# Performance work log

Hardware: AMD Instinct MI355X
Metric: run time of the kernel (lower is better)

The kernel has to match this reference:

```python
import jax, jax.numpy as jnp
import numpy as np

D_MODEL = 1024
NUM_HEADS = 16
HEAD_DIM = D_MODEL // NUM_HEADS


def setup_inputs() -> dict:
    key = jax.random.key(0)
    ks = jax.random.split(key, 9)
    s = 1.0 / np.sqrt(D_MODEL)
    inp = {
        "x": jax.random.normal(ks[0], (4, 2048, D_MODEL), dtype=jnp.float32),
        "wq": jax.random.uniform(ks[1], (D_MODEL, D_MODEL), jnp.float32, -s, s),
        "bq": jax.random.uniform(ks[2], (D_MODEL,), jnp.float32, -s, s),
        "wk": jax.random.uniform(ks[3], (D_MODEL, D_MODEL), jnp.float32, -s, s),
        "bk": jax.random.uniform(ks[4], (D_MODEL,), jnp.float32, -s, s),
        "wv": jax.random.uniform(ks[5], (D_MODEL, D_MODEL), jnp.float32, -s, s),
        "bv": jax.random.uniform(ks[6], (D_MODEL,), jnp.float32, -s, s),
        "wo": jax.random.uniform(ks[7], (D_MODEL, D_MODEL), jnp.float32, -s, s),
        "bo": jax.random.uniform(ks[8], (D_MODEL,), jnp.float32, -s, s),
    }
    return inp


def _split_heads(t):
    # [B, S, D] -> [B, H, S, Dh]
    b, s, _ = t.shape
    return t.reshape(b, s, NUM_HEADS, HEAD_DIM).transpose(0, 2, 1, 3)


def reference(x, wq, bq, wk, bk, wv, bv, wo, bo):
    b, s, _ = x.shape
    q = _split_heads(x @ wq.T + bq)
    k = _split_heads(x @ wk.T + bk)
    v = _split_heads(x @ wv.T + bv)
    scale = 1.0 / np.sqrt(HEAD_DIM).astype(np.float32)
    scores = jnp.einsum('bhqd,bhkd->bhqk', q, k) * scale  # [B,H,S,S]
    probs = jax.nn.softmax(scores, axis=-1)
    ctx = jnp.einsum('bhqk,bhkd->bhqd', probs, v)  # [B,H,S,Dh]
    ctx = ctx.transpose(0, 2, 1, 3).reshape(b, s, D_MODEL)
    return ctx @ wo.T + bo
```

## Files before the change

### kernel.cpp

```cpp
#include <hip/hip_runtime.h>
#include <stdint.h>

typedef short bf16x8 __attribute__((ext_vector_type(8)));
typedef float f32x4 __attribute__((ext_vector_type(4)));

#define D_MODEL 1024
#define NHEAD   16
#define HDIM    64
#define BATCH   4
#define SEQ     2048
#define NTOK    (BATCH * SEQ)

#define BM 128
#define BN 128
#define BK 64

#define LOG2E 1.44269504088896340736f

__device__ __forceinline__ unsigned short f2bf(float f) {
  unsigned int u = __float_as_uint(f);
  u += 0x7fff + ((u >> 16) & 1);
  return (unsigned short)(u >> 16);
}

__device__ __forceinline__ void gload_lds16(const unsigned short* g, unsigned short* l) {
  __builtin_amdgcn_global_load_lds((const __attribute__((address_space(1))) void*)g,
                                   (__attribute__((address_space(3))) void*)l,
                                   16, 0, 0);
}

__global__ __launch_bounds__(256) void cvt_all(
    const float* __restrict__ x, const float* __restrict__ wq,
    const float* __restrict__ wk, const float* __restrict__ wv,
    const float* __restrict__ wo, unsigned short* __restrict__ dst) {
  long i = ((long)blockIdx.x * 256 + threadIdx.x) * 4;
  const float* src; long off;
  if (i < 8388608)       { src = x;  off = 0; }
  else if (i < 9437184)  { src = wq; off = 8388608; }
  else if (i < 10485760) { src = wk; off = 9437184; }
  else if (i < 11534336) { src = wv; off = 10485760; }
  else                   { src = wo; off = 11534336; }
  const float4 v = *(const float4*)(src + (i - off));
  ushort4 o = make_ushort4(f2bf(v.x), f2bf(v.y), f2bf(v.z), f2bf(v.w));
  *(ushort4*)(dst + i) = o;
}

__device__ __forceinline__ void gemm_bt_mainloop(
    const unsigned short* __restrict__ Abase,
    const unsigned short* __restrict__ Bbase,
    int lda, int ldb, int K,
    unsigned short* sA, unsigned short* sB,
    f32x4 acc[4][4]) {
  const int tid = threadIdx.x;
  const int wave = tid >> 6, lane = tid & 63;
  const int ln15 = lane & 15, quad = lane >> 4;
  const int wy = wave >> 1, wx = wave & 1;

#pragma unroll
  for (int mt = 0; mt < 4; ++mt)
#pragma unroll
    for (int nt = 0; nt < 4; ++nt)
      acc[mt][nt] = (f32x4){0.f, 0.f, 0.f, 0.f};

  for (int k0 = 0; k0 < K; k0 += BK) {
    __syncthreads();
#pragma unroll
    for (int i = 0; i < 4; ++i) {
      int chunk = i * 256 + wave * 64 + lane;
      int row = chunk >> 3, c = (chunk & 7) ^ (row & 7);
      gload_lds16(Abase + row * lda + k0 + c * 8, sA + (i * 256 + wave * 64) * 8);
      gload_lds16(Bbase + row * ldb + k0 + c * 8, sB + (i * 256 + wave * 64) * 8);
    }
    __syncthreads();
#pragma unroll
    for (int ks = 0; ks < 2; ++ks) {
      const int swz = ((ks * 4 + quad) ^ (ln15 & 7)) * 8;
      bf16x8 af[4], bfv[4];
#pragma unroll
      for (int t = 0; t < 4; ++t)
        af[t] = *(const bf16x8*)(sA + (64 * wy + 16 * t + ln15) * BK + swz);
#pragma unroll
      for (int t = 0; t < 4; ++t)
        bfv[t] = *(const bf16x8*)(sB + (64 * wx + 16 * t + ln15) * BK + swz);
#pragma unroll
      for (int mt = 0; mt < 4; ++mt)
#pragma unroll
        for (int nt = 0; nt < 4; ++nt)
          acc[mt][nt] = __builtin_amdgcn_mfma_f32_16x16x32_bf16(af[mt], bfv[nt], acc[mt][nt], 0, 0, 0);
    }
  }
}

#define TSTR 136
__global__ __launch_bounds__(256) void qkv_gemm(
    const unsigned short* __restrict__ xb,
    const unsigned short* __restrict__ wqb, const unsigned short* __restrict__ wkb,
    const unsigned short* __restrict__ wvb,
    const float* __restrict__ bq, const float* __restrict__ bk, const float* __restrict__ bv,
    unsigned short* __restrict__ Qb, unsigned short* __restrict__ Kb,
    unsigned short* __restrict__ Vt) {
  const int z = blockIdx.z;
  const unsigned short* W = (z == 0) ? wqb : (z == 1) ? wkb : wvb;
  const float* bias = (z == 0) ? bq : (z == 1) ? bk : bv;
  const int m0 = blockIdx.x * BM, n0 = blockIdx.y * BN;

  __shared__ __align__(16) unsigned char smem[BM * TSTR * 2];
  unsigned short* sA = (unsigned short*)smem;
  unsigned short* sB = (unsigned short*)(smem + BM * BK * 2);
  unsigned short* sT = (unsigned short*)smem;

  f32x4 acc[4][4];
  gemm_bt_mainloop(xb + (size_t)m0 * D_MODEL, W + (size_t)n0 * D_MODEL,
                   D_MODEL, D_MODEL, D_MODEL, sA, sB, acc);

  const int tid = threadIdx.x;
  const int lane = tid & 63, wave = tid >> 6;
  const int ln15 = lane & 15, quad = lane >> 4;
  const int wy = wave >> 1, wx = wave & 1;
  const int b = m0 >> 11;

  if (z == 2) {
    __syncthreads();
#pragma unroll
    for (int mt = 0; mt < 4; ++mt)
#pragma unroll
      for (int nt = 0; nt < 4; ++nt) {
        int j = 64 * wx + 16 * nt + ln15;
        float bj = bias[n0 + j];
#pragma unroll
        for (int r = 0; r < 4; r += 2) {
          int tok = 64 * wy + 16 * mt + quad * 4 + r;
          unsigned int pk = (unsigned int)f2bf(acc[mt][nt][r] + bj) |
                            ((unsigned int)f2bf(acc[mt][nt][r + 1] + bj) << 16);
          *(unsigned int*)(sT + j * TSTR + tok) = pk;
        }
      }
    __syncthreads();
    const int sbase = (m0 & 2047) + (tid & 15) * 8;
#pragma unroll
    for (int i = 0; i < 8; ++i) {
      int j = (tid >> 4) + i * 16;
      int feature = n0 + j;
      int h = feature >> 6, d = feature & 63;
      bf16x8 val = *(const bf16x8*)(sT + j * TSTR + (tid & 15) * 8);
      *(bf16x8*)(Vt + (((size_t)(b * NHEAD + h)) * HDIM + d) * SEQ + sbase) = val;
    }
  } else {
    const float scale = (z == 0) ? 0.125f * LOG2E : 1.0f;
    unsigned short* dst = (z == 0) ? Qb : Kb;
    __syncthreads();
    float bj[4];
#pragma unroll
    for (int nt = 0; nt < 4; ++nt) bj[nt] = bias[n0 + 64 * wx + 16 * nt + ln15];
#pragma unroll
    for (int mt = 0; mt < 4; ++mt)
#pragma unroll
      for (int nt = 0; nt < 4; ++nt)
#pragma unroll
        for (int r = 0; r < 4; ++r) {
          int tok = 64 * wy + 16 * mt + quad * 4 + r;
          int j = 64 * wx + 16 * nt + ln15;
          sT[tok * TSTR + j] = f2bf((acc[mt][nt][r] + bj[nt]) * scale);
        }
    __syncthreads();
    const int srow = m0 & 2047;
#pragma unroll
    for (int i = 0; i < 8; ++i) {
      int tok = (tid >> 4) + i * 16;
      int jj = (tid & 15) * 8;
      bf16x8 val = *(const bf16x8*)(sT + tok * TSTR + jj);
      int feature = n0 + jj;
      int h = feature >> 6, d = feature & 63;
      *(bf16x8*)(dst + (((size_t)(b * NHEAD + h)) * SEQ + srow + tok) * HDIM + d) = val;
    }
  }
}

#define PSTR 72
__global__ __launch_bounds__(256, 4) void attn_kernel(
    const unsigned short* __restrict__ Qb,
    const unsigned short* __restrict__ Kb,
    const unsigned short* __restrict__ Vt,
    unsigned short* __restrict__ ctxb) {
  const int qb = blockIdx.x;
  const int bh = blockIdx.y;
  const int s0 = qb * 128;
  const int tid = threadIdx.x, wave = tid >> 6, lane = tid & 63;
  const int ln15 = lane & 15, quad = lane >> 4;

  __shared__ __align__(16) unsigned short sK[64 * 64], sV[64 * 64], sP[128 * PSTR];

  const unsigned short* Qg = Qb + (size_t)bh * SEQ * HDIM;
  const unsigned short* Kg = Kb + (size_t)bh * SEQ * HDIM;
  const unsigned short* Vg = Vt + (size_t)bh * HDIM * SEQ;

  bf16x8 qf[2][2];
#pragma unroll
  for (int mt = 0; mt < 2; ++mt)
#pragma unroll
    for (int ks = 0; ks < 2; ++ks)
      qf[mt][ks] = *(const bf16x8*)(Qg + (s0 + 32 * wave + 16 * mt + ln15) * HDIM + ks * 32 + quad * 8);

  const int chunk0 = wave * 64 + lane;
  const int row0 = chunk0 >> 3, c0 = (chunk0 & 7) ^ (row0 & 7);
  const int chunk1 = 256 + wave * 64 + lane;
  const int row1 = chunk1 >> 3, c1 = (chunk1 & 7) ^ (row1 & 7);
  const unsigned short* Kp0 = Kg + row0 * HDIM + c0 * 8;
  const unsigned short* Kp1 = Kg + row1 * HDIM + c1 * 8;
  const unsigned short* Vp0 = Vg + row0 * SEQ + c0 * 8;
  const unsigned short* Vp1 = Vg + row1 * SEQ + c1 * 8;
  unsigned short* dK0 = sK + chunk0 * 8;
  unsigned short* dK1 = sK + chunk1 * 8;
  unsigned short* dV0 = sV + chunk0 * 8;
  unsigned short* dV1 = sV + chunk1 * 8;

  float l_part[8];
  f32x4 O[2][4];
#pragma unroll
  for (int i = 0; i < 8; ++i) l_part[i] = 0.f;
#pragma unroll
  for (int mt = 0; mt < 2; ++mt)
#pragma unroll
    for (int dt = 0; dt < 4; ++dt) O[mt][dt] = (f32x4){0.f, 0.f, 0.f, 0.f};

  bf16x8 pk0 = *(const bf16x8*)Kp0;
  bf16x8 pk1 = *(const bf16x8*)Kp1;
  bf16x8 pv0 = *(const bf16x8*)Vp0;
  bf16x8 pv1 = *(const bf16x8*)Vp1;

  for (int t = 0; t < 32; ++t) {
    __syncthreads();
    *(bf16x8*)dK0 = pk0;
    *(bf16x8*)dK1 = pk1;
    *(bf16x8*)dV0 = pv0;
    *(bf16x8*)dV1 = pv1;
    __syncthreads();
    if (t < 31) {
      const int k0 = (t + 1) * 64;
      pk0 = *(const bf16x8*)(Kp0 + k0 * HDIM);
      pk1 = *(const bf16x8*)(Kp1 + k0 * HDIM);
      pv0 = *(const bf16x8*)(Vp0 + k0);
      pv1 = *(const bf16x8*)(Vp1 + k0);
    }

    f32x4 sc[2][4];
#pragma unroll
    for (int mt = 0; mt < 2; ++mt)
#pragma unroll
      for (int nt = 0; nt < 4; ++nt) sc[mt][nt] = (f32x4){0.f, 0.f, 0.f, 0.f};
#pragma unroll
    for (int ks = 0; ks < 2; ++ks) {
      const int swz = ((ks * 4 + quad) ^ (ln15 & 7)) * 8;
#pragma unroll
      for (int nt = 0; nt < 4; ++nt) {
        bf16x8 bk8 = *(const bf16x8*)(sK + (16 * nt + ln15) * 64 + swz);
#pragma unroll
        for (int mt = 0; mt < 2; ++mt)
          sc[mt][nt] = __builtin_amdgcn_mfma_f32_16x16x32_bf16(qf[mt][ks], bk8, sc[mt][nt], 0, 0, 0);
      }
    }

#pragma unroll
    for (int mt = 0; mt < 2; ++mt)
#pragma unroll
      for (int r = 0; r < 4; ++r) {
        float p0 = __builtin_amdgcn_exp2f(sc[mt][0][r]);
        float p1 = __builtin_amdgcn_exp2f(sc[mt][1][r]);
        float p2 = __builtin_amdgcn_exp2f(sc[mt][2][r]);
        float p3 = __builtin_amdgcn_exp2f(sc[mt][3][r]);
        l_part[mt * 4 + r] += (p0 + p1) + (p2 + p3);
        int prow = 32 * wave + 16 * mt + quad * 4 + r;
        sP[prow * PSTR + 0  + ln15] = f2bf(p0);
        sP[prow * PSTR + 16 + ln15] = f2bf(p1);
        sP[prow * PSTR + 32 + ln15] = f2bf(p2);
        sP[prow * PSTR + 48 + ln15] = f2bf(p3);
      }

#pragma unroll
    for (int ks = 0; ks < 2; ++ks) {
      const int swz = ((ks * 4 + quad) ^ (ln15 & 7)) * 8;
      bf16x8 ap[2];
#pragma unroll
      for (int mt = 0; mt < 2; ++mt)
        ap[mt] = *(const bf16x8*)(sP + (32 * wave + 16 * mt + ln15) * PSTR + ks * 32 + quad * 8);
#pragma unroll
      for (int dt = 0; dt < 4; ++dt) {
        bf16x8 bv8 = *(const bf16x8*)(sV + (16 * dt + ln15) * 64 + swz);
#pragma unroll
        for (int mt = 0; mt < 2; ++mt)
          O[mt][dt] = __builtin_amdgcn_mfma_f32_16x16x32_bf16(ap[mt], bv8, O[mt][dt], 0, 0, 0);
      }
    }
  }

  const int b = bh >> 4, h = bh & 15;
#pragma unroll
  for (int mt = 0; mt < 2; ++mt)
#pragma unroll
    for (int r = 0; r < 4; ++r) {
      float l = l_part[mt * 4 + r];
      l += __shfl_xor(l, 1);
      l += __shfl_xor(l, 2);
      l += __shfl_xor(l, 4);
      l += __shfl_xor(l, 8);
      float inv = 1.0f / l;
      int token = b * SEQ + s0 + 32 * wave + 16 * mt + quad * 4 + r;
#pragma unroll
      for (int dt = 0; dt < 4; ++dt)
        ctxb[(size_t)token * D_MODEL + h * HDIM + 16 * dt + ln15] = f2bf(O[mt][dt][r] * inv);
    }
}

__global__ __launch_bounds__(256) void oproj_kernel(
    const unsigned short* __restrict__ ctxb,
    const unsigned short* __restrict__ wob,
    const float* __restrict__ bo,
    float* __restrict__ out) {
  const int m0 = blockIdx.x * BM, n0 = blockIdx.y * BN;
  __shared__ __align__(16) unsigned short sA[BM * BK], sB[BN * BK];
  f32x4 acc[4][4];
  gemm_bt_mainloop(ctxb + (size_t)m0 * D_MODEL, wob + (size_t)n0 * D_MODEL,
                   D_MODEL, D_MODEL, D_MODEL, sA, sB, acc);

  const int lane = threadIdx.x & 63, wave = threadIdx.x >> 6;
  const int ln15 = lane & 15, quad = lane >> 4;
  const int wy = wave >> 1, wx = wave & 1;
#pragma unroll
  for (int mt = 0; mt < 4; ++mt)
#pragma unroll
    for (int nt = 0; nt < 4; ++nt)
#pragma unroll
      for (int r = 0; r < 4; ++r) {
        int n = m0 + 64 * wy + 16 * mt + quad * 4 + r;
        int j = n0 + 64 * wx + 16 * nt + ln15;
        out[(size_t)n * D_MODEL + j] = acc[mt][nt][r] + bo[j];
      }
}

extern "C" void kernel_launch(void* const* d_in, const int* in_sizes, int n_in,
                              void* d_out, int out_size, void* d_ws, size_t ws_size,
                              hipStream_t stream) {
  const float* x  = (const float*)d_in[0];
  const float* wq = (const float*)d_in[1];
  const float* bq = (const float*)d_in[2];
  const float* wk = (const float*)d_in[3];
  const float* bk = (const float*)d_in[4];
  const float* wv = (const float*)d_in[5];
  const float* bv = (const float*)d_in[6];
  const float* wo = (const float*)d_in[7];
  const float* bo = (const float*)d_in[8];
  float* out = (float*)d_out;

  unsigned short* ws   = (unsigned short*)d_ws;
  unsigned short* xb   = ws;
  unsigned short* wqb  = ws + 8388608;
  unsigned short* wkb  = ws + 9437184;
  unsigned short* wvb  = ws + 10485760;
  unsigned short* wob  = ws + 11534336;
  unsigned short* Qb   = ws + 12582912;
  unsigned short* Kb   = ws + 20971520;
  unsigned short* Vtb  = ws + 29360128;
  unsigned short* ctxb = ws + 37748736;

  cvt_all<<<12288, 256, 0, stream>>>(x, wq, wk, wv, wo, ws);

  qkv_gemm<<<dim3(64, 8, 3), 256, 0, stream>>>(xb, wqb, wkb, wvb, bq, bk, bv, Qb, Kb, Vtb);
  attn_kernel<<<dim3(16, 64), 256, 0, stream>>>(Qb, Kb, Vtb, ctxb);
  oproj_kernel<<<dim3(64, 8), 256, 0, stream>>>(ctxb, wob, bo, out);
}
```

Baseline: 280.0 us.

## Use direct global-to-LDS loads in attention and cheaper bf16 rounding

Replaces the register-staged K/V prefetch in the attention loop with global_load_lds DMA-style loads straight into shared memory. The register double-buffering that overlapped the next tile's fetch with compute is dropped. The bf16 conversion switches from round-to-nearest-even to a simpler round-half-up, and the P-tile store address math is hoisted. Removing the prefetch may expose load latency, since loads now happen between barriers with no overlap, and the rounding change slightly alters numerics.

```diff
diff --git a/kernel.cpp b/kernel.cpp
--- a/kernel.cpp
+++ b/kernel.cpp
@@ -17,10 +17,8 @@
 
 #define LOG2E 1.44269504088896340736f
 
-__device__ __forceinline__ unsigned short f2bf(float f) {
-  unsigned int u = __float_as_uint(f);
-  u += 0x7fff + ((u >> 16) & 1);
-  return (unsigned short)(u >> 16);
+__device__ __forceinline__ unsigned short f2bf_fast(float f) {
+  return (unsigned short)((__float_as_uint(f) + 0x8000u) >> 16);
 }
 
 __device__ __forceinline__ void gload_lds16(const unsigned short* g, unsigned short* l) {
@@ -41,7 +39,7 @@
   else if (i < 11534336) { src = wv; off = 10485760; }
   else                   { src = wo; off = 11534336; }
   const float4 v = *(const float4*)(src + (i - off));
-  ushort4 o = make_ushort4(f2bf(v.x), f2bf(v.y), f2bf(v.z), f2bf(v.w));
+  ushort4 o = make_ushort4(f2bf_fast(v.x), f2bf_fast(v.y), f2bf_fast(v.z), f2bf_fast(v.w));
   *(ushort4*)(dst + i) = o;
 }
 
@@ -130,8 +128,8 @@
 #pragma unroll
         for (int r = 0; r < 4; r += 2) {
           int tok = 64 * wy + 16 * mt + quad * 4 + r;
-          unsigned int pk = (unsigned int)f2bf(acc[mt][nt][r] + bj) |
-                            ((unsigned int)f2bf(acc[mt][nt][r + 1] + bj) << 16);
+          unsigned int pk = (unsigned int)f2bf_fast(acc[mt][nt][r] + bj) |
+                            ((unsigned int)f2bf_fast(acc[mt][nt][r + 1] + bj) << 16);
           *(unsigned int*)(sT + j * TSTR + tok) = pk;
         }
       }
@@ -160,7 +158,7 @@
         for (int r = 0; r < 4; ++r) {
           int tok = 64 * wy + 16 * mt + quad * 4 + r;
           int j = 64 * wx + 16 * nt + ln15;
-          sT[tok * TSTR + j] = f2bf((acc[mt][nt][r] + bj[nt]) * scale);
+          sT[tok * TSTR + j] = f2bf_fast((acc[mt][nt][r] + bj[nt]) * scale);
         }
     __syncthreads();
     const int srow = m0 & 2047;
@@ -214,6 +212,8 @@
   unsigned short* dV0 = sV + chunk0 * 8;
   unsigned short* dV1 = sV + chunk1 * 8;
 
+  unsigned short* sPw = sP + (32 * wave + 4 * quad) * PSTR + ln15;
+
   float l_part[8];
   f32x4 O[2][4];
 #pragma unroll
@@ -223,25 +223,13 @@
 #pragma unroll
     for (int dt = 0; dt < 4; ++dt) O[mt][dt] = (f32x4){0.f, 0.f, 0.f, 0.f};
 
-  bf16x8 pk0 = *(const bf16x8*)Kp0;
-  bf16x8 pk1 = *(const bf16x8*)Kp1;
-  bf16x8 pv0 = *(const bf16x8*)Vp0;
-  bf16x8 pv1 = *(const bf16x8*)Vp1;
-
-  for (int t = 0; t < 32; ++t) {
-    __syncthreads();
-    *(bf16x8*)dK0 = pk0;
-    *(bf16x8*)dK1 = pk1;
-    *(bf16x8*)dV0 = pv0;
-    *(bf16x8*)dV1 = pv1;
-    __syncthreads();
-    if (t < 31) {
-      const int k0 = (t + 1) * 64;
-      pk0 = *(const bf16x8*)(Kp0 + k0 * HDIM);
-      pk1 = *(const bf16x8*)(Kp1 + k0 * HDIM);
-      pv0 = *(const bf16x8*)(Vp0 + k0);
-      pv1 = *(const bf16x8*)(Vp1 + k0);
-    }
+  for (int k0 = 0; k0 < SEQ; k0 += 64) {
+    __syncthreads();
+    gload_lds16(Kp0 + k0 * HDIM, dK0);
+    gload_lds16(Kp1 + k0 * HDIM, dK1);
+    gload_lds16(Vp0 + k0, dV0);
+    gload_lds16(Vp1 + k0, dV1);
+    __syncthreads();
 
     f32x4 sc[2][4];
 #pragma unroll
@@ -269,11 +257,11 @@
         float p2 = __builtin_amdgcn_exp2f(sc[mt][2][r]);
         float p3 = __builtin_amdgcn_exp2f(sc[mt][3][r]);
         l_part[mt * 4 + r] += (p0 + p1) + (p2 + p3);
-        int prow = 32 * wave + 16 * mt + quad * 4 + r;
-        sP[prow * PSTR + 0  + ln15] = f2bf(p0);
-        sP[prow * PSTR + 16 + ln15] = f2bf(p1);
-        sP[prow * PSTR + 32 + ln15] = f2bf(p2);
-        sP[prow * PSTR + 48 + ln15] = f2bf(p3);
+        unsigned short* pw = sPw + (16 * mt + r) * PSTR;
+        pw[0]  = (unsigned short)((__float_as_uint(p0) + 0x8000u) >> 16);
+        pw[16] = (unsigned short)((__float_as_uint(p1) + 0x8000u) >> 16);
+        pw[32] = (unsigned short)((__float_as_uint(p2) + 0x8000u) >> 16);
+        pw[48] = (unsigned short)((__float_as_uint(p3) + 0x8000u) >> 16);
       }
 
 #pragma unroll
@@ -307,7 +295,7 @@
       int token = b * SEQ + s0 + 32 * wave + 16 * mt + quad * 4 + r;
 #pragma unroll
       for (int dt = 0; dt < 4; ++dt)
-        ctxb[(size_t)token * D_MODEL + h * HDIM + 16 * dt + ln15] = f2bf(O[mt][dt][r] * inv);
+        ctxb[(size_t)token * D_MODEL + h * HDIM + 16 * dt + ln15] = f2bf_fast(O[mt][dt][r] * inv);
     }
 }
 
```

New measurement: 279.0 us. No clear change (-0.4%).
